# Optimization experiments

Hardware: AMD Instinct MI355X
Metric: run time of the kernel (lower is better)

The kernel has to match this reference:

```python
import jax, jax.numpy as jnp
import numpy as np

N = 150_000      # nodes
E = 4_800_000    # edges (avg degree 32)
F_IN = 3
H = 16           # hidden_dim (module default)
DEPTH = 2        # -> DEPTH-1 = 1 mid layer


def setup_inputs() -> dict:
    key = jax.random.key(0)
    ks = jax.random.split(key, 6)
    x = jax.random.normal(ks[0], (N, F_IN), dtype=jnp.float32)
    edge_index = jax.random.randint(ks[1], (2, E), 0, N, dtype=jnp.int64)
    W_in = jax.random.normal(ks[2], (F_IN, H), dtype=jnp.float32) / np.sqrt(F_IN)
    b_in = jnp.zeros((H,), jnp.float32)
    W_mid = jax.random.normal(ks[3], (DEPTH - 1, H, H), dtype=jnp.float32) / np.sqrt(H)
    b_mid = jnp.zeros((DEPTH - 1, H), jnp.float32)
    W_out = jax.random.normal(ks[4], (H, 1), dtype=jnp.float32) / np.sqrt(H)
    b_out = jnp.zeros((1,), jnp.float32)
    return dict(x=x, edge_index=edge_index, W_in=W_in, b_in=b_in,
                W_mid=W_mid, b_mid=b_mid, W_out=W_out, b_out=b_out)


def _gcn(x, src, dst, norm, W, b):
    # GCNConv: X' = D^{-1/2}(A+I)D^{-1/2} X W + b  (self loops already in src/dst)
    h = x @ W                                   # [N, out]
    msg = h[src] * norm[:, None]                # gather + scale, [E+N, out]
    agg = jax.ops.segment_sum(msg, dst, num_segments=N)  # scatter-add
    return agg + b


def reference(x, edge_index, W_in, b_in, W_mid, b_mid, W_out, b_out):
    loops = jnp.arange(N, dtype=edge_index.dtype)
    src = jnp.concatenate([edge_index[0], loops])
    dst = jnp.concatenate([edge_index[1], loops])
    deg = jax.ops.segment_sum(jnp.ones_like(dst, x.dtype), dst, num_segments=N)
    dinv = jax.lax.rsqrt(jnp.where(deg > 0, deg, 1.0))  # deg >= 1 due to self loops
    norm = dinv[src] * dinv[dst]                # symmetric normalization per edge

    h = jax.nn.relu(_gcn(x, src, dst, norm, W_in, b_in))
    for i in range(DEPTH - 1):                  # dropout p=0.0 -> identity
        h = jax.nn.relu(_gcn(h, src, dst, norm, W_mid[i], b_mid[i]))
    out = _gcn(h, src, dst, norm, W_out, b_out)
    return jax.nn.sigmoid(out)                  # [N, 1]
```

## Files before the change

### kernel.cpp

```cpp
#include <hip/hip_runtime.h>
#include <math.h>

#define NN 150000
#define NE 4800000
#define HD 16
#define NBUCK 586
#define BSH 8
#define NBLK 512
#define CHUNK 9375
#define NSCAN 300032
#define SCANB 293

__device__ __forceinline__ float bf2f(unsigned short u) {
    return __uint_as_float(((unsigned int)u) << 16);
}
__device__ __forceinline__ unsigned short f2bf(float f) {
    unsigned int x = __float_as_uint(f);
    return (unsigned short)((x + 0x7FFFu + ((x >> 16) & 1u)) >> 16);
}


__global__ __launch_bounds__(256) void k_part_count(const int* __restrict__ dst,
                                                    int* __restrict__ C) {
    __shared__ int h[NBUCK];
    for (int i = threadIdx.x; i < NBUCK; i += 256) h[i] = 0;
    __syncthreads();
    int base = blockIdx.x * CHUNK;
    for (int i = threadIdx.x; i < CHUNK; i += 256)
        atomicAdd(&h[dst[base + i] >> BSH], 1);
    __syncthreads();
    for (int i = threadIdx.x; i < NBUCK; i += 256) C[i * NBLK + blockIdx.x] = h[i];
}

__global__ void k_scanA(int* __restrict__ C, int* __restrict__ psum) {
    __shared__ int s[1024];
    int t = threadIdx.x;
    int i = blockIdx.x * 1024 + t;
    int v = C[i];
    s[t] = v;
    __syncthreads();
    for (int off = 1; off < 1024; off <<= 1) {
        int x = (t >= off) ? s[t - off] : 0;
        __syncthreads();
        s[t] += x;
        __syncthreads();
    }
    C[i] = s[t] - v;
    if (t == 1023) psum[blockIdx.x] = s[1023];
}

__global__ void k_scanB(int* __restrict__ psum) {
    __shared__ int s[512];
    int t = threadIdx.x;
    int v = (t < SCANB) ? psum[t] : 0;
    s[t] = v;
    __syncthreads();
    for (int off = 1; off < 512; off <<= 1) {
        int x = (t >= off) ? s[t - off] : 0;
        __syncthreads();
        s[t] += x;
        __syncthreads();
    }
    if (t < SCANB) psum[t] = s[t] - v;
}

__global__ void k_scanC(int* __restrict__ C, const int* __restrict__ psum,
                        int* __restrict__ bstart) {
    int i = blockIdx.x * 1024 + threadIdx.x;
    int v = C[i] + psum[blockIdx.x];
    C[i] = v;
    if ((i & (NBLK - 1)) == 0) bstart[i >> 9] = v;
    if (i == 0) bstart[NBUCK] = NE;
}

__global__ __launch_bounds__(256) void k_part_scatter(const int* __restrict__ src,
                                                      const int* __restrict__ dst,
                                                      const int* __restrict__ C,
                                                      int* __restrict__ packed) {
    __shared__ int cur[NBUCK];
    for (int i = threadIdx.x; i < NBUCK; i += 256) cur[i] = C[i * NBLK + blockIdx.x];
    __syncthreads();
    int base = blockIdx.x * CHUNK;
    for (int i = threadIdx.x; i < CHUNK; i += 256) {
        int s = src[base + i], d = dst[base + i];
        int pos = atomicAdd(&cur[d >> BSH], 1);
        packed[pos] = (s << BSH) | (d & 255);
    }
}

__global__ __launch_bounds__(256) void k_bucket_sort(const int* __restrict__ packed,
                                                     const int* __restrict__ bstart,
                                                     int* __restrict__ row_start,
                                                     float* __restrict__ dinv,
                                                     int* __restrict__ ssrc) {
    __shared__ int hist[256];
    __shared__ int fill[256];
    int b = blockIdx.x;
    int t = threadIdx.x;
    int v0 = b << BSH;
    int nv = min(256, NN - v0);
    int e0 = bstart[b], e1 = bstart[b + 1];
    hist[t] = 0;
    __syncthreads();
    for (int e = e0 + t; e < e1; e += 256)
        atomicAdd(&hist[packed[e] & 255], 1);
    __syncthreads();
    int cv = hist[t];
    __syncthreads();
    for (int off = 1; off < 256; off <<= 1) {
        int x = (t >= off) ? hist[t - off] : 0;
        __syncthreads();
        hist[t] += x;
        __syncthreads();
    }
    int excl = hist[t] - cv;
    if (t < nv) {
        row_start[v0 + t] = e0 + excl;
        fill[t] = e0 + excl;
        dinv[v0 + t] = rsqrtf((float)cv + 1.0f);
    }
    __syncthreads();
    for (int e = e0 + t; e < e1; e += 256) {
        int p = packed[e];
        int pos = atomicAdd(&fill[p & 255], 1);
        ssrc[pos] = p >> BSH;
    }
    if (b == 0 && t == 0) row_start[NN] = NE;
}

__global__ __launch_bounds__(256) void k_transform_in(const float* __restrict__ x,
                                                      const float* __restrict__ W,
                                                      const float* __restrict__ dinv,
                                                      unsigned short* __restrict__ t) {
    int gid = blockIdx.x * blockDim.x + threadIdx.x;
    if (gid >= NN * HD) return;
    int v = gid >> 4, j = gid & 15;
    float s = x[v * 3 + 0] * W[j] + x[v * 3 + 1] * W[HD + j] + x[v * 3 + 2] * W[2 * HD + j];
    t[gid] = f2bf(s * dinv[v]);
}

__global__ __launch_bounds__(256) void k_gather_mid(const int* __restrict__ row_start,
                                                    const int* __restrict__ ssrc,
                                                    const unsigned short* __restrict__ t,
                                                    const float* __restrict__ dinv,
                                                    const float* __restrict__ b,
                                                    const float* __restrict__ W,
                                                    unsigned short* __restrict__ tnext) {
    __shared__ float sW[HD * HD];
    __shared__ float sh[256];
    int tid = threadIdx.x;
    sW[tid] = W[tid];
    int v = blockIdx.x * 16 + (tid >> 4);
    int j = tid & 15;
    int e0 = row_start[v], e1 = row_start[v + 1];
    float sum = 0.0f;
    int e = e0;
    for (; e + 4 <= e1; e += 4) {
        int s0 = ssrc[e], s1 = ssrc[e + 1], s2 = ssrc[e + 2], s3 = ssrc[e + 3];
        sum += bf2f(t[s0 * HD + j]) + bf2f(t[s1 * HD + j])
             + bf2f(t[s2 * HD + j]) + bf2f(t[s3 * HD + j]);
    }
    for (; e < e1; ++e) sum += bf2f(t[ssrc[e] * HD + j]);
    sum += bf2f(t[v * HD + j]);
    float di = dinv[v];
    float h = fmaxf(sum * di + b[j], 0.0f);
    sh[tid] = h;
    __syncthreads();
    int g = tid & 240;
    float o = 0.0f;
#pragma unroll
    for (int k = 0; k < HD; ++k) o += sh[g + k] * sW[k * HD + j];
    tnext[v * HD + j] = f2bf(o * di);
}

__global__ __launch_bounds__(256) void k_gather_out(const int* __restrict__ row_start,
                                                    const int* __restrict__ ssrc,
                                                    const unsigned short* __restrict__ t,
                                                    const float* __restrict__ dinv,
                                                    const float* __restrict__ b,
                                                    const float* __restrict__ Wout,
                                                    float* __restrict__ t3) {
    int tid = threadIdx.x;
    int v = blockIdx.x * 16 + (tid >> 4);
    int j = tid & 15;
    int e0 = row_start[v], e1 = row_start[v + 1];
    float sum = 0.0f;
    int e = e0;
    for (; e + 4 <= e1; e += 4) {
        int s0 = ssrc[e], s1 = ssrc[e + 1], s2 = ssrc[e + 2], s3 = ssrc[e + 3];
        sum += bf2f(t[s0 * HD + j]) + bf2f(t[s1 * HD + j])
             + bf2f(t[s2 * HD + j]) + bf2f(t[s3 * HD + j]);
    }
    for (; e < e1; ++e) sum += bf2f(t[ssrc[e] * HD + j]);
    sum += bf2f(t[v * HD + j]);
    float di = dinv[v];
    float h = fmaxf(sum * di + b[j], 0.0f);
    float d = h * Wout[j];
    d += __shfl_xor(d, 1);
    d += __shfl_xor(d, 2);
    d += __shfl_xor(d, 4);
    d += __shfl_xor(d, 8);
    if (j == 0) t3[v] = d * di;
}

__global__ __launch_bounds__(256) void k_gather_final(const int* __restrict__ row_start,
                                                      const int* __restrict__ ssrc,
                                                      const float* __restrict__ t3,
                                                      const float* __restrict__ dinv,
                                                      const float* __restrict__ b_out,
                                                      float* __restrict__ out) {
    int tid = threadIdx.x;
    int v = blockIdx.x * 16 + (tid >> 4);
    int l = tid & 15;
    int e0 = row_start[v], e1 = row_start[v + 1];
    float sum = 0.0f;
    for (int e = e0 + l; e < e1; e += 16) sum += t3[ssrc[e]];
    sum += __shfl_xor(sum, 1);
    sum += __shfl_xor(sum, 2);
    sum += __shfl_xor(sum, 4);
    sum += __shfl_xor(sum, 8);
    if (l == 0) {
        float z = (sum + t3[v]) * dinv[v] + b_out[0];
        out[v] = 1.0f / (1.0f + expf(-z));
    }
}

extern "C" void kernel_launch(void* const* d_in, const int* in_sizes, int n_in,
                              void* d_out, int out_size, void* d_ws, size_t ws_size,
                              hipStream_t stream) {
    const float* x     = (const float*)d_in[0];
    const int*   ei    = (const int*)d_in[1];
    const float* W_in  = (const float*)d_in[2];
    const float* b_in  = (const float*)d_in[3];
    const float* W_mid = (const float*)d_in[4];
    const float* b_mid = (const float*)d_in[5];
    const float* W_out = (const float*)d_in[6];
    const float* b_out = (const float*)d_in[7];
    float* out = (float*)d_out;

    const int* src = ei;
    const int* dst = ei + NE;

    char* p = (char*)d_ws;
    int*   C         = (int*)p;      p += sizeof(int) * NSCAN;
    int*   psum      = (int*)p;      p += sizeof(int) * 512;
    int*   bstart    = (int*)p;      p += sizeof(int) * (NBUCK + 1);
    int*   row_start = (int*)p;      p += sizeof(int) * (NN + 1);
    float* dinv      = (float*)p;    p += sizeof(float) * NN;
    int*   ssrc      = (int*)p;      p += sizeof(int) * (size_t)NE;
    int*   packed    = (int*)p;      p += sizeof(int) * (size_t)NE;
    unsigned short* tA = (unsigned short*)packed;
    unsigned short* tB = tA + (size_t)NN * HD;
    float* t3          = (float*)(tB + (size_t)NN * HD);

    const int B = 256;
    const int gNH = (NN * HD + B - 1) / B;
    const int gV  = NN / 16;

    k_part_count<<<NBLK, B, 0, stream>>>(dst, C);
    k_scanA<<<SCANB, 1024, 0, stream>>>(C, psum);
    k_scanB<<<1, 512, 0, stream>>>(psum);
    k_scanC<<<SCANB, 1024, 0, stream>>>(C, psum, bstart);
    k_part_scatter<<<NBLK, B, 0, stream>>>(src, dst, C, packed);
    k_bucket_sort<<<NBUCK, B, 0, stream>>>(packed, bstart, row_start, dinv, ssrc);

    k_transform_in<<<gNH, B, 0, stream>>>(x, W_in, dinv, tA);
    k_gather_mid<<<gV, B, 0, stream>>>(row_start, ssrc, tA, dinv, b_in, W_mid, tB);
    k_gather_out<<<gV, B, 0, stream>>>(row_start, ssrc, tB, dinv, b_mid, W_out, t3);
    k_gather_final<<<gV, B, 0, stream>>>(row_start, ssrc, t3, dinv, b_out, out);
}
```

Before: 355.9 us.

## Drop per-node bucket sort; aggregate per bucket via shared-memory atomics

Removes the second-level bucket sort and CSR row_start construction. Each 256-node bucket's edges are now processed directly from the partitioned packed array, accumulating into shared-memory float atomics. Degree computation is fused with the input transform, and the partition pass uses fewer, larger blocks with a swizzled block order. This saves one full pass over the edges plus the ssrc write, at the cost of LDS atomic contention and only 586 blocks in each gather kernel, which may limit occupancy.

```diff
diff --git a/kernel.cpp b/kernel.cpp
--- a/kernel.cpp
+++ b/kernel.cpp
@@ -6,10 +6,10 @@
 #define HD 16
 #define NBUCK 586
 #define BSH 8
-#define NBLK 512
-#define CHUNK 9375
-#define NSCAN 300032
-#define SCANB 293
+#define NBLK 256
+#define CHUNK 18750
+#define NSCAN 150016
+#define SCANB 147
 
 __device__ __forceinline__ float bf2f(unsigned short u) {
     return __uint_as_float(((unsigned int)u) << 16);
@@ -20,23 +20,23 @@
 }
 
 
-__global__ __launch_bounds__(256) void k_part_count(const int* __restrict__ dst,
+__global__ __launch_bounds__(512) void k_part_count(const int* __restrict__ dst,
                                                     int* __restrict__ C) {
     __shared__ int h[NBUCK];
-    for (int i = threadIdx.x; i < NBUCK; i += 256) h[i] = 0;
+    for (int i = threadIdx.x; i < NBUCK; i += 512) h[i] = 0;
     __syncthreads();
     int base = blockIdx.x * CHUNK;
-    for (int i = threadIdx.x; i < CHUNK; i += 256)
+    for (int i = threadIdx.x; i < CHUNK; i += 512)
         atomicAdd(&h[dst[base + i] >> BSH], 1);
     __syncthreads();
-    for (int i = threadIdx.x; i < NBUCK; i += 256) C[i * NBLK + blockIdx.x] = h[i];
+    for (int i = threadIdx.x; i < NBUCK; i += 512) C[i * NBLK + blockIdx.x] = h[i];
 }
 
 __global__ void k_scanA(int* __restrict__ C, int* __restrict__ psum) {
     __shared__ int s[1024];
     int t = threadIdx.x;
     int i = blockIdx.x * 1024 + t;
-    int v = C[i];
+    int v = (i < NSCAN) ? C[i] : 0;
     s[t] = v;
     __syncthreads();
     for (int off = 1; off < 1024; off <<= 1) {
@@ -45,7 +45,7 @@
         s[t] += x;
         __syncthreads();
     }
-    C[i] = s[t] - v;
+    if (i < NSCAN) C[i] = s[t] - v;
     if (t == 1023) psum[blockIdx.x] = s[1023];
 }
 
@@ -67,160 +67,161 @@
 __global__ void k_scanC(int* __restrict__ C, const int* __restrict__ psum,
                         int* __restrict__ bstart) {
     int i = blockIdx.x * 1024 + threadIdx.x;
+    if (i >= NSCAN) return;
     int v = C[i] + psum[blockIdx.x];
     C[i] = v;
-    if ((i & (NBLK - 1)) == 0) bstart[i >> 9] = v;
+    if ((i & (NBLK - 1)) == 0) bstart[i >> BSH] = v;
     if (i == 0) bstart[NBUCK] = NE;
 }
 
-__global__ __launch_bounds__(256) void k_part_scatter(const int* __restrict__ src,
+__global__ __launch_bounds__(512) void k_part_scatter(const int* __restrict__ src,
                                                       const int* __restrict__ dst,
                                                       const int* __restrict__ C,
                                                       int* __restrict__ packed) {
     __shared__ int cur[NBUCK];
-    for (int i = threadIdx.x; i < NBUCK; i += 256) cur[i] = C[i * NBLK + blockIdx.x];
-    __syncthreads();
-    int base = blockIdx.x * CHUNK;
-    for (int i = threadIdx.x; i < CHUNK; i += 256) {
+    int bid = blockIdx.x;
+    int m = ((bid & 7) << 5) | (bid >> 3);
+    for (int i = threadIdx.x; i < NBUCK; i += 512) cur[i] = C[i * NBLK + m];
+    __syncthreads();
+    int base = m * CHUNK;
+    for (int i = threadIdx.x; i < CHUNK; i += 512) {
         int s = src[base + i], d = dst[base + i];
         int pos = atomicAdd(&cur[d >> BSH], 1);
         packed[pos] = (s << BSH) | (d & 255);
     }
 }
 
-__global__ __launch_bounds__(256) void k_bucket_sort(const int* __restrict__ packed,
-                                                     const int* __restrict__ bstart,
-                                                     int* __restrict__ row_start,
-                                                     float* __restrict__ dinv,
-                                                     int* __restrict__ ssrc) {
-    __shared__ int hist[256];
-    __shared__ int fill[256];
-    int b = blockIdx.x;
-    int t = threadIdx.x;
+__global__ __launch_bounds__(512) void k_deg_transform(const int* __restrict__ packed,
+                                                       const int* __restrict__ bstart,
+                                                       const float* __restrict__ x,
+                                                       const float* __restrict__ W,
+                                                       float* __restrict__ dinv,
+                                                       unsigned short* __restrict__ tA) {
+    __shared__ int deg[256];
+    __shared__ float sdinv[256];
+    __shared__ float sx[256 * 3];
+    __shared__ float sW[3 * HD];
+    int b = blockIdx.x, t = threadIdx.x;
     int v0 = b << BSH;
     int nv = min(256, NN - v0);
+    if (t < 256) deg[t] = 0;
+    if (t < 3 * HD) sW[t] = W[t];
+    __syncthreads();
     int e0 = bstart[b], e1 = bstart[b + 1];
-    hist[t] = 0;
-    __syncthreads();
-    for (int e = e0 + t; e < e1; e += 256)
-        atomicAdd(&hist[packed[e] & 255], 1);
-    __syncthreads();
-    int cv = hist[t];
-    __syncthreads();
-    for (int off = 1; off < 256; off <<= 1) {
-        int x = (t >= off) ? hist[t - off] : 0;
-        __syncthreads();
-        hist[t] += x;
-        __syncthreads();
-    }
-    int excl = hist[t] - cv;
-    if (t < nv) {
-        row_start[v0 + t] = e0 + excl;
-        fill[t] = e0 + excl;
-        dinv[v0 + t] = rsqrtf((float)cv + 1.0f);
-    }
-    __syncthreads();
-    for (int e = e0 + t; e < e1; e += 256) {
-        int p = packed[e];
-        int pos = atomicAdd(&fill[p & 255], 1);
-        ssrc[pos] = p >> BSH;
-    }
-    if (b == 0 && t == 0) row_start[NN] = NE;
-}
-
-__global__ __launch_bounds__(256) void k_transform_in(const float* __restrict__ x,
-                                                      const float* __restrict__ W,
-                                                      const float* __restrict__ dinv,
-                                                      unsigned short* __restrict__ t) {
-    int gid = blockIdx.x * blockDim.x + threadIdx.x;
-    if (gid >= NN * HD) return;
-    int v = gid >> 4, j = gid & 15;
-    float s = x[v * 3 + 0] * W[j] + x[v * 3 + 1] * W[HD + j] + x[v * 3 + 2] * W[2 * HD + j];
-    t[gid] = f2bf(s * dinv[v]);
-}
-
-__global__ __launch_bounds__(256) void k_gather_mid(const int* __restrict__ row_start,
-                                                    const int* __restrict__ ssrc,
+    for (int e = e0 + t; e < e1; e += 512)
+        atomicAdd(&deg[packed[e] & 255], 1);
+    for (int i = t; i < nv * 3; i += 512) sx[i] = x[v0 * 3 + i];
+    __syncthreads();
+    if (t < 256) {
+        float di = rsqrtf((float)(deg[t] + 1));
+        sdinv[t] = di;
+        if (t < nv) dinv[v0 + t] = di;
+    }
+    __syncthreads();
+    for (int idx = t; idx < nv * HD; idx += 512) {
+        int n = idx >> 4, j = idx & 15;
+        float s = sx[n * 3 + 0] * sW[j] + sx[n * 3 + 1] * sW[HD + j] + sx[n * 3 + 2] * sW[2 * HD + j];
+        tA[(size_t)(v0 + n) * HD + j] = f2bf(s * sdinv[n]);
+    }
+}
+
+__global__ __launch_bounds__(512) void k_gather_mid(const int* __restrict__ packed,
+                                                    const int* __restrict__ bstart,
                                                     const unsigned short* __restrict__ t,
                                                     const float* __restrict__ dinv,
                                                     const float* __restrict__ b,
                                                     const float* __restrict__ W,
                                                     unsigned short* __restrict__ tnext) {
+    __shared__ float acc[256 * HD];
     __shared__ float sW[HD * HD];
-    __shared__ float sh[256];
-    int tid = threadIdx.x;
-    sW[tid] = W[tid];
-    int v = blockIdx.x * 16 + (tid >> 4);
-    int j = tid & 15;
-    int e0 = row_start[v], e1 = row_start[v + 1];
-    float sum = 0.0f;
-    int e = e0;
-    for (; e + 4 <= e1; e += 4) {
-        int s0 = ssrc[e], s1 = ssrc[e + 1], s2 = ssrc[e + 2], s3 = ssrc[e + 3];
-        sum += bf2f(t[s0 * HD + j]) + bf2f(t[s1 * HD + j])
-             + bf2f(t[s2 * HD + j]) + bf2f(t[s3 * HD + j]);
-    }
-    for (; e < e1; ++e) sum += bf2f(t[ssrc[e] * HD + j]);
-    sum += bf2f(t[v * HD + j]);
-    float di = dinv[v];
-    float h = fmaxf(sum * di + b[j], 0.0f);
-    sh[tid] = h;
-    __syncthreads();
-    int g = tid & 240;
-    float o = 0.0f;
+    __shared__ float sb[HD];
+    int bk = blockIdx.x, tid = threadIdx.x;
+    int v0 = bk << BSH;
+    int nv = min(256, NN - v0);
+    for (int i = tid; i < 256 * HD; i += 512) acc[i] = 0.0f;
+    if (tid < HD * HD) sW[tid] = W[tid];
+    if (tid < HD) sb[tid] = b[tid];
+    __syncthreads();
+    int e0 = bstart[bk], e1 = bstart[bk + 1];
+    int g = tid >> 4, j = tid & 15;
+    for (int e = e0 + g; e < e1; e += 32) {
+        int p = packed[e];
+        atomicAdd(&acc[(p & 255) * HD + j], bf2f(t[(size_t)(p >> BSH) * HD + j]));
+    }
+    __syncthreads();
+    for (int n = g; n < nv; n += 32) {
+        int v = v0 + n;
+        float sum = acc[n * HD + j] + bf2f(t[(size_t)v * HD + j]);
+        acc[n * HD + j] = fmaxf(sum * dinv[v] + sb[j], 0.0f);
+    }
+    __syncthreads();
+    for (int n = g; n < nv; n += 32) {
+        int v = v0 + n;
+        float o = 0.0f;
 #pragma unroll
-    for (int k = 0; k < HD; ++k) o += sh[g + k] * sW[k * HD + j];
-    tnext[v * HD + j] = f2bf(o * di);
-}
-
-__global__ __launch_bounds__(256) void k_gather_out(const int* __restrict__ row_start,
-                                                    const int* __restrict__ ssrc,
+        for (int k = 0; k < HD; ++k) o += acc[n * HD + k] * sW[k * HD + j];
+        tnext[(size_t)v * HD + j] = f2bf(o * dinv[v]);
+    }
+}
+
+__global__ __launch_bounds__(512) void k_gather_out(const int* __restrict__ packed,
+                                                    const int* __restrict__ bstart,
                                                     const unsigned short* __restrict__ t,
                                                     const float* __restrict__ dinv,
                                                     const float* __restrict__ b,
                                                     const float* __restrict__ Wout,
                                                     float* __restrict__ t3) {
-    int tid = threadIdx.x;
-    int v = blockIdx.x * 16 + (tid >> 4);
-    int j = tid & 15;
-    int e0 = row_start[v], e1 = row_start[v + 1];
-    float sum = 0.0f;
-    int e = e0;
-    for (; e + 4 <= e1; e += 4) {
-        int s0 = ssrc[e], s1 = ssrc[e + 1], s2 = ssrc[e + 2], s3 = ssrc[e + 3];
-        sum += bf2f(t[s0 * HD + j]) + bf2f(t[s1 * HD + j])
-             + bf2f(t[s2 * HD + j]) + bf2f(t[s3 * HD + j]);
-    }
-    for (; e < e1; ++e) sum += bf2f(t[ssrc[e] * HD + j]);
-    sum += bf2f(t[v * HD + j]);
-    float di = dinv[v];
-    float h = fmaxf(sum * di + b[j], 0.0f);
-    float d = h * Wout[j];
-    d += __shfl_xor(d, 1);
-    d += __shfl_xor(d, 2);
-    d += __shfl_xor(d, 4);
-    d += __shfl_xor(d, 8);
-    if (j == 0) t3[v] = d * di;
-}
-
-__global__ __launch_bounds__(256) void k_gather_final(const int* __restrict__ row_start,
-                                                      const int* __restrict__ ssrc,
+    __shared__ float acc[256 * HD];
+    __shared__ float sW[HD];
+    __shared__ float sb[HD];
+    int bk = blockIdx.x, tid = threadIdx.x;
+    int v0 = bk << BSH;
+    int nv = min(256, NN - v0);
+    for (int i = tid; i < 256 * HD; i += 512) acc[i] = 0.0f;
+    if (tid < HD) { sW[tid] = Wout[tid]; sb[tid] = b[tid]; }
+    __syncthreads();
+    int e0 = bstart[bk], e1 = bstart[bk + 1];
+    int g = tid >> 4, j = tid & 15;
+    for (int e = e0 + g; e < e1; e += 32) {
+        int p = packed[e];
+        atomicAdd(&acc[(p & 255) * HD + j], bf2f(t[(size_t)(p >> BSH) * HD + j]));
+    }
+    __syncthreads();
+    for (int n = g; n < nv; n += 32) {
+        int v = v0 + n;
+        float di = dinv[v];
+        float sum = acc[n * HD + j] + bf2f(t[(size_t)v * HD + j]);
+        float h = fmaxf(sum * di + sb[j], 0.0f);
+        float d = h * sW[j];
+        d += __shfl_xor(d, 1);
+        d += __shfl_xor(d, 2);
+        d += __shfl_xor(d, 4);
+        d += __shfl_xor(d, 8);
+        if (j == 0) t3[v] = d * di;
+    }
+}
+
+__global__ __launch_bounds__(512) void k_gather_final(const int* __restrict__ packed,
+                                                      const int* __restrict__ bstart,
                                                       const float* __restrict__ t3,
                                                       const float* __restrict__ dinv,
                                                       const float* __restrict__ b_out,
                                                       float* __restrict__ out) {
-    int tid = threadIdx.x;
-    int v = blockIdx.x * 16 + (tid >> 4);
-    int l = tid & 15;
-    int e0 = row_start[v], e1 = row_start[v + 1];
-    float sum = 0.0f;
-    for (int e = e0 + l; e < e1; e += 16) sum += t3[ssrc[e]];
-    sum += __shfl_xor(sum, 1);
-    sum += __shfl_xor(sum, 2);
-    sum += __shfl_xor(sum, 4);
-    sum += __shfl_xor(sum, 8);
-    if (l == 0) {
-        float z = (sum + t3[v]) * dinv[v] + b_out[0];
+    __shared__ float facc[256];
+    int bk = blockIdx.x, tid = threadIdx.x;
+    int v0 = bk << BSH;
+    int nv = min(256, NN - v0);
+    if (tid < 256) facc[tid] = 0.0f;
+    __syncthreads();
+    int e0 = bstart[bk], e1 = bstart[bk + 1];
+    for (int e = e0 + tid; e < e1; e += 512) {
+        int p = packed[e];
+        atomicAdd(&facc[p & 255], t3[p >> BSH]);
+    }
+    __syncthreads();
+    if (tid < nv) {
+        int v = v0 + tid;
+        float z = (facc[tid] + t3[v]) * dinv[v] + b_out[0];
         out[v] = 1.0f / (1.0f + expf(-z));
     }
 }
@@ -242,30 +243,24 @@
     const int* dst = ei + NE;
 
     char* p = (char*)d_ws;
-    int*   C         = (int*)p;      p += sizeof(int) * NSCAN;
-    int*   psum      = (int*)p;      p += sizeof(int) * 512;
-    int*   bstart    = (int*)p;      p += sizeof(int) * (NBUCK + 1);
-    int*   row_start = (int*)p;      p += sizeof(int) * (NN + 1);
-    float* dinv      = (float*)p;    p += sizeof(float) * NN;
-    int*   ssrc      = (int*)p;      p += sizeof(int) * (size_t)NE;
-    int*   packed    = (int*)p;      p += sizeof(int) * (size_t)NE;
-    unsigned short* tA = (unsigned short*)packed;
-    unsigned short* tB = tA + (size_t)NN * HD;
-    float* t3          = (float*)(tB + (size_t)NN * HD);
-
-    const int B = 256;
-    const int gNH = (NN * HD + B - 1) / B;
-    const int gV  = NN / 16;
-
-    k_part_count<<<NBLK, B, 0, stream>>>(dst, C);
+    int*   C      = (int*)p;     p += sizeof(int) * NSCAN;
+    int*   psum   = (int*)p;     p += sizeof(int) * 160;
+    int*   bstart = (int*)p;     p += sizeof(int) * (NBUCK + 2);
+    float* dinv   = (float*)p;   p += sizeof(float) * NN;
+    int*   packed = (int*)p;     p += sizeof(int) * (size_t)NE;
+    unsigned short* tA = (unsigned short*)p; p += sizeof(unsigned short) * (size_t)NN * HD;
+    unsigned short* tB = (unsigned short*)p; p += sizeof(unsigned short) * (size_t)NN * HD;
+    float* t3     = (float*)p;   p += sizeof(float) * NN;
+
+    k_part_count<<<NBLK, 512, 0, stream>>>(dst, C);
     k_scanA<<<SCANB, 1024, 0, stream>>>(C, psum);
     k_scanB<<<1, 512, 0, stream>>>(psum);
     k_scanC<<<SCANB, 1024, 0, stream>>>(C, psum, bstart);
-    k_part_scatter<<<NBLK, B, 0, stream>>>(src, dst, C, packed);
-    k_bucket_sort<<<NBUCK, B, 0, stream>>>(packed, bstart, row_start, dinv, ssrc);
-
-    k_transform_in<<<gNH, B, 0, stream>>>(x, W_in, dinv, tA);
-    k_gather_mid<<<gV, B, 0, stream>>>(row_start, ssrc, tA, dinv, b_in, W_mid, tB);
-    k_gather_out<<<gV, B, 0, stream>>>(row_start, ssrc, tB, dinv, b_mid, W_out, t3);
-    k_gather_final<<<gV, B, 0, stream>>>(row_start, ssrc, t3, dinv, b_out, out);
-}
+    k_part_scatter<<<NBLK, 512, 0, stream>>>(src, dst, C, packed);
+
+    k_deg_transform<<<NBUCK, 512, 0, stream>>>(packed, bstart, x, W_in, dinv, tA);
+
+    k_gather_mid<<<NBUCK, 512, 0, stream>>>(packed, bstart, tA, dinv, b_in, W_mid, tB);
+    k_gather_out<<<NBUCK, 512, 0, stream>>>(packed, bstart, tB, dinv, b_mid, W_out, t3);
+    k_gather_final<<<NBUCK, 512, 0, stream>>>(packed, bstart, t3, dinv, b_out, out);
+}
```

New measurement: 1.226 ms. +244.4%, slower.

## Use two half-waves per node in gathers and halve partition block count

Applied to the files above, without the earlier changes.

The gather kernels now assign 32 lanes per node instead of 16. Each half-wavefront sums alternate edges and the halves are combined with a shuffle, which doubles memory-level parallelism on the irregular neighbor loads. The partition phase uses 256 blocks of 512 threads with larger chunks, and the scan gains bounds checks. Scatter block IDs are remapped to interleave chunk order. The changes add thread overhead and leave idle lanes in the dense transform step of gather_mid.

```diff
diff --git a/kernel.cpp b/kernel.cpp
--- a/kernel.cpp
+++ b/kernel.cpp
@@ -6,10 +6,10 @@
 #define HD 16
 #define NBUCK 586
 #define BSH 8
-#define NBLK 512
-#define CHUNK 9375
-#define NSCAN 300032
-#define SCANB 293
+#define NBLK 256
+#define CHUNK 18750
+#define NSCAN 150016
+#define SCANB 147
 
 __device__ __forceinline__ float bf2f(unsigned short u) {
     return __uint_as_float(((unsigned int)u) << 16);
@@ -20,23 +20,23 @@
 }
 
 
-__global__ __launch_bounds__(256) void k_part_count(const int* __restrict__ dst,
+__global__ __launch_bounds__(512) void k_part_count(const int* __restrict__ dst,
                                                     int* __restrict__ C) {
     __shared__ int h[NBUCK];
-    for (int i = threadIdx.x; i < NBUCK; i += 256) h[i] = 0;
+    for (int i = threadIdx.x; i < NBUCK; i += 512) h[i] = 0;
     __syncthreads();
     int base = blockIdx.x * CHUNK;
-    for (int i = threadIdx.x; i < CHUNK; i += 256)
+    for (int i = threadIdx.x; i < CHUNK; i += 512)
         atomicAdd(&h[dst[base + i] >> BSH], 1);
     __syncthreads();
-    for (int i = threadIdx.x; i < NBUCK; i += 256) C[i * NBLK + blockIdx.x] = h[i];
+    for (int i = threadIdx.x; i < NBUCK; i += 512) C[i * NBLK + blockIdx.x] = h[i];
 }
 
 __global__ void k_scanA(int* __restrict__ C, int* __restrict__ psum) {
     __shared__ int s[1024];
     int t = threadIdx.x;
     int i = blockIdx.x * 1024 + t;
-    int v = C[i];
+    int v = (i < NSCAN) ? C[i] : 0;
     s[t] = v;
     __syncthreads();
     for (int off = 1; off < 1024; off <<= 1) {
@@ -45,7 +45,7 @@
         s[t] += x;
         __syncthreads();
     }
-    C[i] = s[t] - v;
+    if (i < NSCAN) C[i] = s[t] - v;
     if (t == 1023) psum[blockIdx.x] = s[1023];
 }
 
@@ -67,21 +67,24 @@
 __global__ void k_scanC(int* __restrict__ C, const int* __restrict__ psum,
                         int* __restrict__ bstart) {
     int i = blockIdx.x * 1024 + threadIdx.x;
+    if (i >= NSCAN) return;
     int v = C[i] + psum[blockIdx.x];
     C[i] = v;
-    if ((i & (NBLK - 1)) == 0) bstart[i >> 9] = v;
+    if ((i & (NBLK - 1)) == 0) bstart[i >> BSH] = v;
     if (i == 0) bstart[NBUCK] = NE;
 }
 
-__global__ __launch_bounds__(256) void k_part_scatter(const int* __restrict__ src,
+__global__ __launch_bounds__(512) void k_part_scatter(const int* __restrict__ src,
                                                       const int* __restrict__ dst,
                                                       const int* __restrict__ C,
                                                       int* __restrict__ packed) {
     __shared__ int cur[NBUCK];
-    for (int i = threadIdx.x; i < NBUCK; i += 256) cur[i] = C[i * NBLK + blockIdx.x];
-    __syncthreads();
-    int base = blockIdx.x * CHUNK;
-    for (int i = threadIdx.x; i < CHUNK; i += 256) {
+    int bid = blockIdx.x;
+    int m = ((bid & 7) << 5) | (bid >> 3);
+    for (int i = threadIdx.x; i < NBUCK; i += 512) cur[i] = C[i * NBLK + m];
+    __syncthreads();
+    int base = m * CHUNK;
+    for (int i = threadIdx.x; i < CHUNK; i += 512) {
         int s = src[base + i], d = dst[base + i];
         int pos = atomicAdd(&cur[d >> BSH], 1);
         packed[pos] = (s << BSH) | (d & 255);
@@ -139,7 +142,7 @@
     t[gid] = f2bf(s * dinv[v]);
 }
 
-__global__ __launch_bounds__(256) void k_gather_mid(const int* __restrict__ row_start,
+__global__ __launch_bounds__(512) void k_gather_mid(const int* __restrict__ row_start,
                                                     const int* __restrict__ ssrc,
                                                     const unsigned short* __restrict__ t,
                                                     const float* __restrict__ dinv,
@@ -147,33 +150,41 @@
                                                     const float* __restrict__ W,
                                                     unsigned short* __restrict__ tnext) {
     __shared__ float sW[HD * HD];
-    __shared__ float sh[256];
+    __shared__ float sh[16 * HD];
     int tid = threadIdx.x;
-    sW[tid] = W[tid];
-    int v = blockIdx.x * 16 + (tid >> 4);
-    int j = tid & 15;
+    if (tid < HD * HD) sW[tid] = W[tid];
+    int node = tid >> 5;
+    int lane = tid & 31;
+    int j = lane & 15;
+    int half = lane >> 4;
+    int v = blockIdx.x * 16 + node;
     int e0 = row_start[v], e1 = row_start[v + 1];
     float sum = 0.0f;
-    int e = e0;
-    for (; e + 4 <= e1; e += 4) {
-        int s0 = ssrc[e], s1 = ssrc[e + 1], s2 = ssrc[e + 2], s3 = ssrc[e + 3];
-        sum += bf2f(t[s0 * HD + j]) + bf2f(t[s1 * HD + j])
-             + bf2f(t[s2 * HD + j]) + bf2f(t[s3 * HD + j]);
-    }
-    for (; e < e1; ++e) sum += bf2f(t[ssrc[e] * HD + j]);
-    sum += bf2f(t[v * HD + j]);
-    float di = dinv[v];
-    float h = fmaxf(sum * di + b[j], 0.0f);
-    sh[tid] = h;
-    __syncthreads();
-    int g = tid & 240;
-    float o = 0.0f;
+    int e = e0 + half;
+    for (; e + 6 < e1; e += 8) {
+        int s0 = ssrc[e], s1 = ssrc[e + 2], s2 = ssrc[e + 4], s3 = ssrc[e + 6];
+        sum += bf2f(t[(size_t)s0 * HD + j]) + bf2f(t[(size_t)s1 * HD + j])
+             + bf2f(t[(size_t)s2 * HD + j]) + bf2f(t[(size_t)s3 * HD + j]);
+    }
+    for (; e < e1; e += 2) sum += bf2f(t[(size_t)ssrc[e] * HD + j]);
+    if (half == 0) sum += bf2f(t[(size_t)v * HD + j]);
+    sum += __shfl_xor(sum, 16);
+    if (half == 0) {
+        float h = fmaxf(sum * dinv[v] + b[j], 0.0f);
+        sh[node * HD + j] = h;
+    }
+    __syncthreads();
+    if (tid < 256) {
+        int n = tid >> 4, jj = tid & 15;
+        int vv = blockIdx.x * 16 + n;
+        float o = 0.0f;
 #pragma unroll
-    for (int k = 0; k < HD; ++k) o += sh[g + k] * sW[k * HD + j];
-    tnext[v * HD + j] = f2bf(o * di);
-}
-
-__global__ __launch_bounds__(256) void k_gather_out(const int* __restrict__ row_start,
+        for (int k = 0; k < HD; ++k) o += sh[n * HD + k] * sW[k * HD + jj];
+        tnext[(size_t)vv * HD + jj] = f2bf(o * dinv[vv]);
+    }
+}
+
+__global__ __launch_bounds__(512) void k_gather_out(const int* __restrict__ row_start,
                                                     const int* __restrict__ ssrc,
                                                     const unsigned short* __restrict__ t,
                                                     const float* __restrict__ dinv,
@@ -181,18 +192,22 @@
                                                     const float* __restrict__ Wout,
                                                     float* __restrict__ t3) {
     int tid = threadIdx.x;
-    int v = blockIdx.x * 16 + (tid >> 4);
-    int j = tid & 15;
+    int node = tid >> 5;
+    int lane = tid & 31;
+    int j = lane & 15;
+    int half = lane >> 4;
+    int v = blockIdx.x * 16 + node;
     int e0 = row_start[v], e1 = row_start[v + 1];
     float sum = 0.0f;
-    int e = e0;
-    for (; e + 4 <= e1; e += 4) {
-        int s0 = ssrc[e], s1 = ssrc[e + 1], s2 = ssrc[e + 2], s3 = ssrc[e + 3];
-        sum += bf2f(t[s0 * HD + j]) + bf2f(t[s1 * HD + j])
-             + bf2f(t[s2 * HD + j]) + bf2f(t[s3 * HD + j]);
-    }
-    for (; e < e1; ++e) sum += bf2f(t[ssrc[e] * HD + j]);
-    sum += bf2f(t[v * HD + j]);
+    int e = e0 + half;
+    for (; e + 6 < e1; e += 8) {
+        int s0 = ssrc[e], s1 = ssrc[e + 2], s2 = ssrc[e + 4], s3 = ssrc[e + 6];
+        sum += bf2f(t[(size_t)s0 * HD + j]) + bf2f(t[(size_t)s1 * HD + j])
+             + bf2f(t[(size_t)s2 * HD + j]) + bf2f(t[(size_t)s3 * HD + j]);
+    }
+    for (; e < e1; e += 2) sum += bf2f(t[(size_t)ssrc[e] * HD + j]);
+    if (half == 0) sum += bf2f(t[(size_t)v * HD + j]);
+    sum += __shfl_xor(sum, 16);
     float di = dinv[v];
     float h = fmaxf(sum * di + b[j], 0.0f);
     float d = h * Wout[j];
@@ -200,7 +215,7 @@
     d += __shfl_xor(d, 2);
     d += __shfl_xor(d, 4);
     d += __shfl_xor(d, 8);
-    if (j == 0) t3[v] = d * di;
+    if (lane == 0) t3[v] = d * di;
 }
 
 __global__ __launch_bounds__(256) void k_gather_final(const int* __restrict__ row_start,
@@ -243,8 +258,8 @@
 
     char* p = (char*)d_ws;
     int*   C         = (int*)p;      p += sizeof(int) * NSCAN;
-    int*   psum      = (int*)p;      p += sizeof(int) * 512;
-    int*   bstart    = (int*)p;      p += sizeof(int) * (NBUCK + 1);
+    int*   psum      = (int*)p;      p += sizeof(int) * 160;
+    int*   bstart    = (int*)p;      p += sizeof(int) * (NBUCK + 2);
     int*   row_start = (int*)p;      p += sizeof(int) * (NN + 1);
     float* dinv      = (float*)p;    p += sizeof(float) * NN;
     int*   ssrc      = (int*)p;      p += sizeof(int) * (size_t)NE;
@@ -253,19 +268,18 @@
     unsigned short* tB = tA + (size_t)NN * HD;
     float* t3          = (float*)(tB + (size_t)NN * HD);
 
-    const int B = 256;
-    const int gNH = (NN * HD + B - 1) / B;
+    const int gNH = (NN * HD + 255) / 256;
     const int gV  = NN / 16;
 
-    k_part_count<<<NBLK, B, 0, stream>>>(dst, C);
+    k_part_count<<<NBLK, 512, 0, stream>>>(dst, C);
     k_scanA<<<SCANB, 1024, 0, stream>>>(C, psum);
     k_scanB<<<1, 512, 0, stream>>>(psum);
     k_scanC<<<SCANB, 1024, 0, stream>>>(C, psum, bstart);
-    k_part_scatter<<<NBLK, B, 0, stream>>>(src, dst, C, packed);
-    k_bucket_sort<<<NBUCK, B, 0, stream>>>(packed, bstart, row_start, dinv, ssrc);
-
-    k_transform_in<<<gNH, B, 0, stream>>>(x, W_in, dinv, tA);
-    k_gather_mid<<<gV, B, 0, stream>>>(row_start, ssrc, tA, dinv, b_in, W_mid, tB);
-    k_gather_out<<<gV, B, 0, stream>>>(row_start, ssrc, tB, dinv, b_mid, W_out, t3);
-    k_gather_final<<<gV, B, 0, stream>>>(row_start, ssrc, t3, dinv, b_out, out);
-}
+    k_part_scatter<<<NBLK, 512, 0, stream>>>(src, dst, C, packed);
+    k_bucket_sort<<<NBUCK, 256, 0, stream>>>(packed, bstart, row_start, dinv, ssrc);
+
+    k_transform_in<<<gNH, 256, 0, stream>>>(x, W_in, dinv, tA);
+    k_gather_mid<<<gV, 512, 0, stream>>>(row_start, ssrc, tA, dinv, b_in, W_mid, tB);
+    k_gather_out<<<gV, 512, 0, stream>>>(row_start, ssrc, tB, dinv, b_mid, W_out, t3);
+    k_gather_final<<<gV, 256, 0, stream>>>(row_start, ssrc, t3, dinv, b_out, out);
+}
```

Measured after the change: 366.9 us. 1.03x slower.
